# Kernel optimization log

Hardware: AMD Instinct MI355X
Metric: run time of the kernel (lower is better)

Reference implementation:

```python
import jax, jax.numpy as jnp
import numpy as np

B = 4096
D = 512
N_CLASSES = 100
TEMPERATURE = 0.5


def setup_inputs() -> dict:
    key = jax.random.key(0)
    k1, k2, k3 = jax.random.split(key, 3)
    emb_i = jax.random.normal(k1, (B, D), dtype=jnp.float32)
    emb_j = jax.random.normal(k2, (B, D), dtype=jnp.float32)
    target = jax.random.randint(k3, (B,), 0, N_CLASSES, dtype=jnp.int64)
    return {"emb_i": emb_i, "emb_j": emb_j, "target": target}


def _l2_normalize(x, eps=1e-12):
    # matches torch F.normalize(dim=1): x / max(||x||, eps)
    n = jnp.sqrt(jnp.sum(x * x, axis=1, keepdims=True))
    return x / jnp.maximum(n, eps)


def reference(emb_i, emb_j, target):
    size = emb_i.shape[0]          # B
    n2 = 2 * size                  # 2B
    t = jnp.float32(TEMPERATURE)

    z_i = _l2_normalize(emb_i)
    z_j = _l2_normalize(emb_j)
    reps = jnp.concatenate([z_i, z_j], axis=0)                 # [2B, D]
    sim = jnp.matmul(reps, reps.T)                             # [2B, 2B]

    # positives: diag at offsets +B and -B
    sim_ij = jnp.diagonal(sim, offset=size)                    # [B]
    sim_ji = jnp.diagonal(sim, offset=-size)                   # [B]
    positives = jnp.concatenate([sim_ij, sim_ji], axis=0)      # [2B]
    nominator = jnp.exp(positives / t)

    idx = jnp.arange(n2)
    labels = jnp.concatenate([target, target])                 # [2B]
    # sample_mask: zero where same label AND |i-j| != B (also zeros the diagonal)
    same_label = labels[:, None] == labels[None, :]
    not_pos_pair = jnp.abs(idx[:, None] - idx[None, :]) != size
    sample_mask = jnp.where(same_label & not_pos_pair, 0.0, 1.0).astype(jnp.float32)
    # negatives_mask: ~eye
    neg_mask = 1.0 - jnp.eye(n2, dtype=jnp.float32)

    denom = jnp.sum(sample_mask * neg_mask * jnp.exp(sim / t), axis=1)  # [2B]
    loss_partial = -jnp.log(nominator / (denom + 1e-7))
    loss = jnp.sum(loss_partial) / n2
    return loss
```

## Files before the change

### kernel.cpp

```cpp
#include <hip/hip_runtime.h>
#include <hip/hip_bf16.h>
#include <cstdint>

#define B_SIZE 4096
#define TWO_B  8192
#define DIM    512
#define NBLK   1056
#define EXP_SCALE 2.8853900817779268f

typedef __attribute__((ext_vector_type(4))) float f32x4;

#define WAITVM(n) __builtin_amdgcn_s_waitcnt(0xF70 | (n))
#define BARRIER() __builtin_amdgcn_s_barrier()

__device__ __forceinline__ void async16(const void* g, void* l) {
    __builtin_amdgcn_global_load_lds(
        (const __attribute__((address_space(1))) unsigned int*)g,
        (__attribute__((address_space(3))) unsigned int*)l,
        16, 0, 0);
}

__global__ __launch_bounds__(256) void norm_pos_kernel(
    const float* __restrict__ emb_i, const float* __restrict__ emb_j,
    unsigned char* __restrict__ reps, float* __restrict__ pos,
    float* __restrict__ out)
{
    __shared__ float sc[3][4];
    int b = blockIdx.x, t = threadIdx.x;
    if (b == 0 && t == 0) out[0] = 0.0f;

    const float2* ri = (const float2*)(emb_i + (size_t)b * DIM);
    const float2* rj = (const float2*)(emb_j + (size_t)b * DIM);
    float2 xi = ri[t], xj = rj[t];
    float si = xi.x * xi.x + xi.y * xi.y;
    float sj = xj.x * xj.x + xj.y * xj.y;
    #pragma unroll
    for (int o = 32; o > 0; o >>= 1) { si += __shfl_down(si, o, 64); sj += __shfl_down(sj, o, 64); }
    int lane = t & 63, w = t >> 6;
    if (lane == 0) { sc[0][w] = si; sc[1][w] = sj; }
    __syncthreads();
    float ni2 = sc[0][0] + sc[0][1] + sc[0][2] + sc[0][3];
    float nj2 = sc[1][0] + sc[1][1] + sc[1][2] + sc[1][3];
    float rni = 1.0f / fmaxf(sqrtf(ni2), 1e-12f);
    float rnj = 1.0f / fmaxf(sqrtf(nj2), 1e-12f);
    float zix = xi.x * rni, ziy = xi.y * rni;
    float zjx = xj.x * rnj, zjy = xj.y * rnj;
    int pki = __builtin_amdgcn_cvt_pk_fp8_f32(zix, ziy, 0, false);
    int pkj = __builtin_amdgcn_cvt_pk_fp8_f32(zjx, zjy, 0, false);
    ((unsigned short*)(reps + (size_t)b * DIM))[t]            = (unsigned short)pki;
    ((unsigned short*)(reps + (size_t)(b + B_SIZE) * DIM))[t] = (unsigned short)pkj;
    float d = zix * zjx + ziy * zjy;
    #pragma unroll
    for (int o = 32; o > 0; o >>= 1) d += __shfl_down(d, o, 64);
    if (lane == 0) sc[2][w] = d;
    __syncthreads();
    if (t == 0) pos[b] = sc[2][0] + sc[2][1] + sc[2][2] + sc[2][3];
}

#define BK 64
#define KITERS 8
#define RSTR 20

__global__ __launch_bounds__(512, 4) void sim_denom_kernel(
    const unsigned char* __restrict__ reps,
    const int* __restrict__ target,
    float* __restrict__ part)
{
    __shared__ __align__(16) unsigned char SMEM[49152];
    unsigned char* As0 = SMEM;
    unsigned char* As1 = SMEM + 16384;
    unsigned char* Bs0 = SMEM + 32768;
    unsigned char* Bs1 = SMEM + 40960;

    int t = threadIdx.x;
    int id0 = blockIdx.x;
    int id = (id0 & 7) * 132 + (id0 >> 3);

    const int bA[10]   = {0,0,0,0,1,1,1,2,2,3};
    const int bB[10]   = {0,1,2,3,1,2,3,2,3,3};
    const int boff[11] = {0,72,200,328,456,528,656,784,856,984,1056};
    int s = 0;
    while (boff[s + 1] <= id) s++;
    int l = id - boff[s];
    int I, J;
    if (bA[s] == bB[s]) {
        int r = 0;
        while ((r + 1) * (16 - r) <= l) r++;
        I = bA[s] * 8 + r;
        J = bB[s] * 16 + 2 * r + (l - r * (17 - r));
    } else { I = bA[s] * 8 + (l >> 4); J = bB[s] * 16 + (l & 15); }

    int brow = I * 256;
    int bcol = J * 128;

    int wave = t >> 6, lane = t & 63;
    int wr = wave >> 1, wc = wave & 1;
    int quad = lane >> 4, lm = lane & 15;

    f32x4 acc[4][4];
    #pragma unroll
    for (int i = 0; i < 4; i++)
        #pragma unroll
        for (int j = 0; j < 4; j++) acc[i][j] = (f32x4)0.0f;

    int srow = t >> 2;
    int sp   = (t & 3) ^ ((srow ^ (srow >> 2)) & 3);
    const unsigned char* gA = reps + (size_t)(brow + srow) * DIM + sp * 16;
    const unsigned char* gB = reps + (size_t)(bcol + srow) * DIM + sp * 16;

    auto stage = [&](unsigned char* Ab, unsigned char* Bb, int k0) {
        async16(gA + k0, Ab + t * 16);
        async16(gA + k0 + 128 * DIM, Ab + t * 16 + 8192);
        async16(gB + k0, Bb + t * 16);
    };
    auto compute = [&](const unsigned char* Ab, const unsigned char* Bb) {
        #pragma unroll
        for (int ss = 0; ss < 2; ss++) {
            long af[4], bf[4];
            #pragma unroll
            for (int mi = 0; mi < 4; mi++) {
                int rl = wr * 64 + mi * 16 + lm;
                int p = (ss * 2 + (quad >> 1)) ^ ((rl ^ (rl >> 2)) & 3);
                af[mi] = *(const long*)(Ab + rl * 64 + p * 16 + (quad & 1) * 8);
            }
            #pragma unroll
            for (int ni = 0; ni < 4; ni++) {
                int cl = wc * 64 + ni * 16 + lm;
                int p = (ss * 2 + (quad >> 1)) ^ ((cl ^ (cl >> 2)) & 3);
                bf[ni] = *(const long*)(Bb + cl * 64 + p * 16 + (quad & 1) * 8);
            }
            #pragma unroll
            for (int mi = 0; mi < 4; mi++)
                #pragma unroll
                for (int ni = 0; ni < 4; ni++)
                    acc[mi][ni] = __builtin_amdgcn_mfma_f32_16x16x32_fp8_fp8(
                        af[mi], bf[ni], acc[mi][ni], 0, 0, 0);
        }
    };

    stage(As0, Bs0, 0);
    stage(As1, Bs1, BK);

    #pragma unroll
    for (int k = 0; k < KITERS; k++) {
        unsigned char* Ac = (k & 1) ? As1 : As0;
        unsigned char* Bc = (k & 1) ? Bs1 : Bs0;
        if (k < KITERS - 1) WAITVM(3); else WAITVM(0);
        BARRIER();
        compute(Ac, Bc);
        BARRIER();
        if (k + 2 < KITERS) stage(Ac, Bc, (k + 2) * BK);
    }

    int h = wr >> 1;
    int rtile = 2 * I + h;
    bool haspos = (J - rtile == 32);
    int labc[4];
    #pragma unroll
    for (int ni = 0; ni < 4; ni++)
        labc[ni] = target[(bcol + wc * 64 + ni * 16 + lm) & (B_SIZE - 1)];

    float* red0    = (float*)SMEM;
    float* red1    = (float*)(SMEM + 20480);
    float* red_col = (float*)(SMEM + 40960);
    float* redw    = wc ? red1 : red0;

    float colacc[4] = {0.f, 0.f, 0.f, 0.f};
    #pragma unroll
    for (int mi = 0; mi < 4; mi++) {
        #pragma unroll
        for (int r = 0; r < 4; r++) {
            int rl = wr * 64 + mi * 16 + quad * 4 + r;
            int labr = target[(brow + rl) & (B_SIZE - 1)];
            float rowacc = 0.0f;
            #pragma unroll
            for (int ni = 0; ni < 4; ni++) {
                int cl = wc * 64 + ni * 16 + lm;
                bool pospair = haspos && ((rl & 127) == cl);
                bool masked = (labr == labc[ni]) && !pospair;
                float e = masked ? 0.0f
                                 : __builtin_amdgcn_exp2f(acc[mi][ni][r] * EXP_SCALE);
                rowacc += e;
                colacc[ni] += e;
            }
            redw[rl * RSTR + lm] = rowacc;
        }
    }
    #pragma unroll
    for (int ni = 0; ni < 4; ni++) {
        float c = colacc[ni];
        c += __shfl_xor(c, 16, 64);
        c += __shfl_xor(c, 32, 64);
        if (quad == 0) red_col[h * 256 + (wr & 1) * 128 + wc * 64 + ni * 16 + lm] = c;
    }
    BARRIER();
    if (t < 256) {
        int th = t >> 7;
        if (2 * I + th <= J) {
            const f32x4* r0 = (const f32x4*)(red0 + t * RSTR);
            const f32x4* r1 = (const f32x4*)(red1 + t * RSTR);
            f32x4 v = r0[0] + r0[1] + r0[2] + r0[3]
                    + r1[0] + r1[1] + r1[2] + r1[3];
            part[(size_t)J * TWO_B + brow + t] = v[0] + v[1] + v[2] + v[3];
        }
    } else if (t < 512) {
        int c = t - 256;
        int ch = c >> 7, cc = c & 127;
        int rt = 2 * I + ch;
        if (rt < J) {
            float cs = red_col[ch * 256 + cc] + red_col[ch * 256 + 128 + cc];
            part[(size_t)rt * TWO_B + bcol + cc] = cs;
        }
    }
}

__global__ __launch_bounds__(256) void loss_kernel(
    const float* __restrict__ part, const float* __restrict__ pos,
    float* __restrict__ out)
{
    __shared__ float sc[4];
    int t = threadIdx.x, b = blockIdx.x;
    int i = b * 256 + t;
    float s = 0.0f;
    #pragma unroll
    for (int x = 0; x < 64; x++) s += part[(size_t)x * TWO_B + i];
    float v = logf(s + 1e-7f);
    float p = (i < B_SIZE) ? pos[i] : 0.0f;
    float v2 = v - 4.0f * p;
    #pragma unroll
    for (int o = 32; o > 0; o >>= 1) v2 += __shfl_down(v2, o, 64);
    int lane = t & 63, w = t >> 6;
    if (lane == 0) sc[w] = v2;
    __syncthreads();
    if (t == 0) atomicAdd(out, (sc[0] + sc[1] + sc[2] + sc[3]) * (1.0f / (float)TWO_B));
}

extern "C" void kernel_launch(void* const* d_in, const int* in_sizes, int n_in,
                              void* d_out, int out_size, void* d_ws, size_t ws_size,
                              hipStream_t stream)
{
    const float* emb_i  = (const float*)d_in[0];
    const float* emb_j  = (const float*)d_in[1];
    const int*   target = (const int*)d_in[2];
    float* out = (float*)d_out;

    char* ws = (char*)d_ws;
    unsigned char* reps = (unsigned char*)ws;
    float* pos   = (float*)(ws + (size_t)TWO_B * DIM);
    float* part  = (float*)(ws + (size_t)TWO_B * DIM + B_SIZE * 4);

    norm_pos_kernel<<<B_SIZE, 256, 0, stream>>>(emb_i, emb_j, reps, pos, out);
    sim_denom_kernel<<<NBLK, 512, 0, stream>>>(reps, target, part);
    loss_kernel<<<TWO_B / 256, 256, 0, stream>>>(part, pos, out);
}
```

Measured before the change: 108.7 us.

## Switch similarity GEMM from fp8 MFMA to int8 MFMA with symmetric quantization

Normalized embeddings are now quantized to int8 (scale 127) instead of fp8, and the similarity GEMM uses the 16x16x64 i8 MFMA with int32 accumulators. Each K-tile takes one 16-byte LDS load per fragment and one MFMA instead of two 8-byte loads and two fp8 MFMAs, which halves MFMA issue count and LDS instructions. The exponent scale is folded to undo the 127^2 factor. This trades fp8's dynamic range for uniform int8 quantization, which changes numerical error in the dot products.

```diff
diff --git a/kernel.cpp b/kernel.cpp
--- a/kernel.cpp
+++ b/kernel.cpp
@@ -6,9 +6,11 @@
 #define TWO_B  8192
 #define DIM    512
 #define NBLK   1056
-#define EXP_SCALE 2.8853900817779268f
+#define IEXP_SCALE 1.7889578968877387e-4f
+#define EXP_SCALE  2.8853900817779268f
 
 typedef __attribute__((ext_vector_type(4))) float f32x4;
+typedef __attribute__((ext_vector_type(4))) int   i32x4;
 
 #define WAITVM(n) __builtin_amdgcn_s_waitcnt(0xF70 | (n))
 #define BARRIER() __builtin_amdgcn_s_barrier()
@@ -45,10 +47,12 @@
     float rnj = 1.0f / fmaxf(sqrtf(nj2), 1e-12f);
     float zix = xi.x * rni, ziy = xi.y * rni;
     float zjx = xj.x * rnj, zjy = xj.y * rnj;
-    int pki = __builtin_amdgcn_cvt_pk_fp8_f32(zix, ziy, 0, false);
-    int pkj = __builtin_amdgcn_cvt_pk_fp8_f32(zjx, zjy, 0, false);
-    ((unsigned short*)(reps + (size_t)b * DIM))[t]            = (unsigned short)pki;
-    ((unsigned short*)(reps + (size_t)(b + B_SIZE) * DIM))[t] = (unsigned short)pkj;
+    int qix = __float2int_rn(zix * 127.0f), qiy = __float2int_rn(ziy * 127.0f);
+    int qjx = __float2int_rn(zjx * 127.0f), qjy = __float2int_rn(zjy * 127.0f);
+    ((unsigned short*)(reps + (size_t)b * DIM))[t] =
+        (unsigned short)((qix & 0xFF) | ((qiy & 0xFF) << 8));
+    ((unsigned short*)(reps + (size_t)(b + B_SIZE) * DIM))[t] =
+        (unsigned short)((qjx & 0xFF) | ((qjy & 0xFF) << 8));
     float d = zix * zjx + ziy * zjy;
     #pragma unroll
     for (int o = 32; o > 0; o >>= 1) d += __shfl_down(d, o, 64);
@@ -97,11 +101,11 @@
     int wr = wave >> 1, wc = wave & 1;
     int quad = lane >> 4, lm = lane & 15;
 
-    f32x4 acc[4][4];
+    i32x4 acc[4][4];
     #pragma unroll
     for (int i = 0; i < 4; i++)
         #pragma unroll
-        for (int j = 0; j < 4; j++) acc[i][j] = (f32x4)0.0f;
+        for (int j = 0; j < 4; j++) acc[i][j] = (i32x4)0;
 
     int srow = t >> 2;
     int sp   = (t & 3) ^ ((srow ^ (srow >> 2)) & 3);
@@ -114,27 +118,22 @@
         async16(gB + k0, Bb + t * 16);
     };
     auto compute = [&](const unsigned char* Ab, const unsigned char* Bb) {
-        #pragma unroll
-        for (int ss = 0; ss < 2; ss++) {
-            long af[4], bf[4];
+        i32x4 bf[4];
+        #pragma unroll
+        for (int ni = 0; ni < 4; ni++) {
+            int cl = wc * 64 + ni * 16 + lm;
+            int p = quad ^ ((cl ^ (cl >> 2)) & 3);
+            bf[ni] = *(const i32x4*)(Bb + cl * 64 + p * 16);
+        }
+        #pragma unroll
+        for (int mi = 0; mi < 4; mi++) {
+            int rl = wr * 64 + mi * 16 + lm;
+            int p = quad ^ ((rl ^ (rl >> 2)) & 3);
+            i32x4 af = *(const i32x4*)(Ab + rl * 64 + p * 16);
             #pragma unroll
-            for (int mi = 0; mi < 4; mi++) {
-                int rl = wr * 64 + mi * 16 + lm;
-                int p = (ss * 2 + (quad >> 1)) ^ ((rl ^ (rl >> 2)) & 3);
-                af[mi] = *(const long*)(Ab + rl * 64 + p * 16 + (quad & 1) * 8);
-            }
-            #pragma unroll
-            for (int ni = 0; ni < 4; ni++) {
-                int cl = wc * 64 + ni * 16 + lm;
-                int p = (ss * 2 + (quad >> 1)) ^ ((cl ^ (cl >> 2)) & 3);
-                bf[ni] = *(const long*)(Bb + cl * 64 + p * 16 + (quad & 1) * 8);
-            }
-            #pragma unroll
-            for (int mi = 0; mi < 4; mi++)
-                #pragma unroll
-                for (int ni = 0; ni < 4; ni++)
-                    acc[mi][ni] = __builtin_amdgcn_mfma_f32_16x16x32_fp8_fp8(
-                        af[mi], bf[ni], acc[mi][ni], 0, 0, 0);
+            for (int ni = 0; ni < 4; ni++)
+                acc[mi][ni] = __builtin_amdgcn_mfma_i32_16x16x64_i8(
+                    af, bf[ni], acc[mi][ni], 0, 0, 0);
         }
     };
 
@@ -179,7 +178,8 @@
                 bool pospair = haspos && ((rl & 127) == cl);
                 bool masked = (labr == labc[ni]) && !pospair;
                 float e = masked ? 0.0f
-                                 : __builtin_amdgcn_exp2f(acc[mi][ni][r] * EXP_SCALE);
+                                 : __builtin_amdgcn_exp2f(
+                                       (float)acc[mi][ni][r] * IEXP_SCALE);
                 rowacc += e;
                 colacc[ni] += e;
             }
```

Measured after the change: 106.5 us. 2.1% less time.
